# Optimization experiments

Hardware: AMD Instinct MI355X
Metric: run time of the kernel (lower is better)

## Reference

```python
import jax, jax.numpy as jnp
import numpy as np

B, S, D = 1, 4096, 1024
H, W = 16, 512            # heads, window_size
HD = D // H               # head_dim = 64


def setup_inputs() -> dict:
    key = jax.random.key(0)
    k1, k2, k3 = jax.random.split(key, 3)
    x = jax.random.normal(k1, (B, S, D), dtype=jnp.float32)
    w_qkv = jax.random.normal(k2, (D, 3 * D), dtype=jnp.float32) * 0.02
    w_out = jax.random.normal(k3, (D, D), dtype=jnp.float32) * 0.02
    return {"x": x, "w_qkv": w_qkv, "w_out": w_out}


def reference(x, w_qkv, w_out):
    b, s, d = x.shape
    qkv = x @ w_qkv                                   # [B,S,3D]
    q, k, v = jnp.split(qkv, 3, axis=-1)
    to_heads = lambda t: t.reshape(b, s, H, HD).transpose(0, 2, 1, 3)  # [B,H,S,hd]
    q, k, v = map(to_heads, (q, k, v))

    C = s // W                                        # number of chunks
    qc = q.reshape(b, H, C, W, HD)                    # [B,H,C,W,hd]
    kc = k.reshape(b, H, C, W, HD)
    vc = v.reshape(b, H, C, W, HD)

    # each chunk attends to [previous chunk, current chunk] of K/V (2W keys)
    zero = jnp.zeros_like(kc[:, :, :1])
    k_prev = jnp.concatenate([zero, kc[:, :, :-1]], axis=2)
    v_prev = jnp.concatenate([jnp.zeros_like(vc[:, :, :1]), vc[:, :, :-1]], axis=2)
    kcat = jnp.concatenate([k_prev, kc], axis=3)      # [B,H,C,2W,hd]
    vcat = jnp.concatenate([v_prev, vc], axis=3)

    scores = jnp.einsum('bhcqd,bhckd->bhcqk', qc, kcat) / (HD ** 0.5)

    # mask: causal (abs q_pos >= abs k_pos) and k_pos >= 0 (first chunk has no prev)
    wq = jnp.arange(W)
    jk = jnp.arange(2 * W)
    ci = jnp.arange(C)
    causal = (wq[:, None] + W) >= jk[None, :]                    # [W,2W]
    valid = (ci[:, None, None] * W + jk[None, None, :] - W) >= 0  # [C,1,2W]
    mask = causal[None] & valid                                   # [C,W,2W]

    scores = jnp.where(mask[None, None], scores, -jnp.inf)
    attn = jax.nn.softmax(scores, axis=-1)
    out = jnp.einsum('bhcqk,bhckd->bhcqd', attn, vcat)            # [B,H,C,W,hd]
    out = out.reshape(b, H, s, HD).transpose(0, 2, 1, 3).reshape(b, s, d)
    return out @ w_out
```

## Files before the change

### kernel.cpp

```cpp
#include <hip/hip_runtime.h>

typedef __attribute__((ext_vector_type(8))) short short8;
typedef __attribute__((ext_vector_type(4))) float f32x4;
typedef __attribute__((ext_vector_type(4))) unsigned short us4;
typedef unsigned short u16;

__device__ __forceinline__ u16 f2bf(float f) {
  unsigned int u = __float_as_uint(f);
  u += 0x7fffu + ((u >> 16) & 1u);
  return (u16)(u >> 16);
}

__device__ __forceinline__ void gld16(const void* g, void* l) {
  __builtin_amdgcn_global_load_lds((const __attribute__((address_space(1))) void*)g,
                                   (__attribute__((address_space(3))) void*)l, 16, 0, 0);
}

__global__ __launch_bounds__(256) void cast_f32_to_bf16(const float* __restrict__ in,
                                                        u16* __restrict__ out, int n8) {
  int i = blockIdx.x * 256 + threadIdx.x;
  if (i >= n8) return;
  const f32x4* p = (const f32x4*)in;
  f32x4 a = p[i * 2];
  f32x4 b = p[i * 2 + 1];
  short8 o;
#pragma unroll
  for (int j = 0; j < 4; ++j) o[j] = (short)f2bf(a[j]);
#pragma unroll
  for (int j = 0; j < 4; ++j) o[4 + j] = (short)f2bf(b[j]);
  ((short8*)out)[i] = o;
}

__global__ __launch_bounds__(256) void transpose_cast(const float* __restrict__ w,
                                                      u16* __restrict__ wT, int K, int N) {
  __shared__ float tile[32][33];
  int n0 = blockIdx.x * 32, k0 = blockIdx.y * 32;
  int r = threadIdx.x >> 5;
  int c = threadIdx.x & 31;
#pragma unroll
  for (int i = 0; i < 4; ++i)
    tile[r + i * 8][c] = w[(size_t)(k0 + r + i * 8) * N + n0 + c];
  __syncthreads();
#pragma unroll
  for (int i = 0; i < 4; ++i)
    wT[(size_t)(n0 + r + i * 8) * K + k0 + c] = f2bf(tile[c][r + i * 8]);
}

__global__ __launch_bounds__(256) void transpose_v(const u16* __restrict__ vh,
                                                   u16* __restrict__ vt) {
  __shared__ u16 tile[32][33];
  const int s0 = blockIdx.x * 32, d0 = blockIdx.y * 32, h = blockIdx.z;
  const long hb = (long)h * 4096 * 64;
  const long hb2 = (long)h * 64 * 4096;
  const int r = threadIdx.x >> 5, c = threadIdx.x & 31;
#pragma unroll
  for (int i = 0; i < 4; ++i)
    tile[r + i * 8][c] = vh[hb + (long)(s0 + r + i * 8) * 64 + d0 + c];
  __syncthreads();
#pragma unroll
  for (int i = 0; i < 4; ++i)
    vt[hb2 + (long)(d0 + r + i * 8) * 4096 + s0 + c] = tile[c][r + i * 8];
}

template <int MODE, int BM, int BN>
__global__ __launch_bounds__(256) void gemm_bf16(
    const u16* __restrict__ A, const u16* __restrict__ Bt, float* __restrict__ C,
    u16* __restrict__ q_out, u16* __restrict__ k_out, u16* __restrict__ v_out,
    int M, int N, int K) {
  __shared__ __align__(16) u16 As[BM][64];
  __shared__ __align__(16) u16 Bs[BN][64];
  constexpr int MW = BM / 32;
  constexpr int NW = BN / 32;
  const int t = threadIdx.x;
  const int lane = t & 63;
  const int wid = t >> 6;
  const int wm = wid >> 1, wn = wid & 1;
  const int l15 = lane & 15, lhi = lane >> 4;

  const int nbx = gridDim.x;
  const int bid = blockIdx.y * nbx + blockIdx.x;
  const int cpx = (nbx * gridDim.y) >> 3;
  const int wg = (bid & 7) * cpx + (bid >> 3);
  const int m0 = (wg / nbx) * BM;
  const int n0 = (wg % nbx) * BN;

  const int srow = lane >> 3;
  const int scol = ((lane & 7) ^ (lane >> 3)) * 8;

  f32x4 acc[MW][NW];
#pragma unroll
  for (int mi = 0; mi < MW; ++mi)
#pragma unroll
    for (int ni = 0; ni < NW; ++ni) acc[mi][ni] = (f32x4){0.f, 0.f, 0.f, 0.f};

  for (int k0 = 0; k0 < K; k0 += 64) {
    __syncthreads();
#pragma unroll
    for (int i = 0; i < MW; ++i) {
      int cch = wid * MW + i;
      int row = cch * 8 + srow;
      const u16* src = (MODE == 2)
          ? &A[((size_t)(k0 >> 6) * 4096 + m0 + row) * 64 + scol]
          : &A[(size_t)(m0 + row) * K + k0 + scol];
      gld16(src, &As[cch * 8][0]);
    }
#pragma unroll
    for (int i = 0; i < NW; ++i) {
      int cch = wid * NW + i;
      int row = cch * 8 + srow;
      gld16(&Bt[(size_t)(n0 + row) * K + k0 + scol], &Bs[cch * 8][0]);
    }
    __syncthreads();
#pragma unroll
    for (int kc = 0; kc < 2; ++kc) {
      short8 af[MW], bf[NW];
#pragma unroll
      for (int mi = 0; mi < MW; ++mi) {
        int row = wm * (BM / 2) + mi * 16 + l15;
        af[mi] = *(const short8*)&As[row][((kc * 4 + lhi) ^ (l15 & 7)) * 8];
      }
#pragma unroll
      for (int ni = 0; ni < NW; ++ni) {
        int row = wn * (BN / 2) + ni * 16 + l15;
        bf[ni] = *(const short8*)&Bs[row][((kc * 4 + lhi) ^ (l15 & 7)) * 8];
      }
#pragma unroll
      for (int mi = 0; mi < MW; ++mi)
#pragma unroll
        for (int ni = 0; ni < NW; ++ni)
          acc[mi][ni] = __builtin_amdgcn_mfma_f32_16x16x32_bf16(af[mi], bf[ni], acc[mi][ni], 0, 0, 0);
    }
  }

  const float SCQ = 0.18033688011112042f;
#pragma unroll
  for (int mi = 0; mi < MW; ++mi)
#pragma unroll
    for (int ni = 0; ni < NW; ++ni)
#pragma unroll
      for (int r = 0; r < 4; ++r) {
        int row = m0 + wm * (BM / 2) + mi * 16 + lhi * 4 + r;
        int col = n0 + wn * (BN / 2) + ni * 16 + l15;
        float val = acc[mi][ni][r];
        if constexpr (MODE == 1) {
          int which = col >> 10;
          int d = col & 1023;
          int hh = d >> 6, hd = d & 63;
          if (which == 0)      q_out[((size_t)hh * 4096 + row) * 64 + hd] = f2bf(val * SCQ);
          else if (which == 1) k_out[((size_t)hh * 4096 + row) * 64 + hd] = f2bf(val);
          else                 v_out[((size_t)hh * 4096 + row) * 64 + hd] = f2bf(val);
        } else {
          C[(size_t)row * N + col] = val;
        }
      }
}

__global__ __launch_bounds__(512) void attn_kernel(
    const u16* __restrict__ qh,
    const u16* __restrict__ kh,
    const u16* __restrict__ vt,
    u16* __restrict__ outh) {
  __shared__ __align__(16) u16 Ks[2][64][64];
  __shared__ __align__(16) u16 Vt[2][64][64];
  __shared__ __align__(16) unsigned int Pl[8][16][37];

  const int t = threadIdx.x;
  const int lane = t & 63;
  const int w = t >> 6;
  const int l15 = lane & 15;
  const int lhi = lane >> 4;

  const int bid = blockIdx.x;
  const int wk = (bid & 7) * 64 + (bid >> 3);
  const int qt = wk & 3, c = (wk >> 2) & 7, h = wk >> 5;

  const long head_base = (long)h * 4096 * 64;
  const int q0 = qt * 128;
  const long q_gbase = head_base + (long)(c * 512 + q0) * 64;

  short8 qf[2];
#pragma unroll
  for (int kc = 0; kc < 2; ++kc)
    qf[kc] = *(const short8*)&qh[q_gbase + (long)(w * 16 + l15) * 64 + kc * 32 + lhi * 8];

  float m_run = -1e30f, l_run = 0.f;
  f32x4 acc_o[4];
#pragma unroll
  for (int nd = 0; nd < 4; ++nd) acc_o[nd] = (f32x4){0.f, 0.f, 0.f, 0.f};

  const int kt_start = (c == 0) ? 8 : 0;
  const int kt_end = 2 * qt + 9;
  const long kv_base = head_base + ((long)c - 1) * 512 * 64;
  const long vt_hb = (long)h * 64 * 4096 + ((long)c - 1) * 512;

  const int srow = lane >> 3;
  const int sunit8 = ((lane & 7) ^ (lane >> 3)) * 8;

  {
    const int j0 = kt_start * 64;
    gld16(&kh[kv_base + (long)(j0 + w * 8 + srow) * 64 + sunit8], &Ks[0][w * 8][0]);
    gld16(&vt[vt_hb + (long)(w * 8 + srow) * 4096 + j0 + sunit8], &Vt[0][w * 8][0]);
  }
  __syncthreads();

  int cur = 0;
  for (int kt = kt_start; kt <= kt_end; ++kt) {
    const int j0 = kt * 64;
    const int nxt = cur ^ 1;

    if (kt < kt_end) {
      const int j0n = j0 + 64;
      gld16(&kh[kv_base + (long)(j0n + w * 8 + srow) * 64 + sunit8], &Ks[nxt][w * 8][0]);
      gld16(&vt[vt_hb + (long)(w * 8 + srow) * 4096 + j0n + sunit8], &Vt[nxt][w * 8][0]);
    }

    const bool active = (j0 <= q0 + w * 16 + 15 + 512);
    if (active) {
      f32x4 sa[4];
#pragma unroll
      for (int ni = 0; ni < 4; ++ni) sa[ni] = (f32x4){0.f, 0.f, 0.f, 0.f};
#pragma unroll
      for (int kc = 0; kc < 2; ++kc) {
        short8 kf[4];
#pragma unroll
        for (int ni = 0; ni < 4; ++ni) {
          int row = ni * 16 + l15;
          kf[ni] = *(const short8*)&Ks[cur][row][((kc * 4 + lhi) ^ (l15 & 7)) * 8];
        }
#pragma unroll
        for (int ni = 0; ni < 4; ++ni)
          sa[ni] = __builtin_amdgcn_mfma_f32_16x16x32_bf16(kf[ni], qf[kc], sa[ni], 0, 0, 0);
      }

      const int qloc = q0 + w * 16 + l15;
      if (j0 + 63 > q0 + w * 16 + 512) {
        const int lim = qloc + 512 - j0 - 4 * lhi;
#pragma unroll
        for (int ni = 0; ni < 4; ++ni)
#pragma unroll
          for (int r = 0; r < 4; ++r)
            if (16 * ni + r > lim) sa[ni][r] = -1e30f;
      }
      float v[16];
#pragma unroll
      for (int ni = 0; ni < 4; ++ni)
#pragma unroll
        for (int r = 0; r < 4; ++r) v[ni * 4 + r] = sa[ni][r];
#pragma unroll
      for (int s = 8; s >= 1; s >>= 1)
#pragma unroll
        for (int k = 0; k < s; ++k) v[k] = fmaxf(v[k], v[k + s]);
      float tm = v[0];
      tm = fmaxf(tm, __shfl_xor(tm, 16, 64));
      tm = fmaxf(tm, __shfl_xor(tm, 32, 64));

      float mn = fmaxf(m_run, tm);
      float corr = __builtin_amdgcn_exp2f(m_run - mn);
      m_run = mn;

      float ps[16];
#pragma unroll
      for (int ni = 0; ni < 4; ++ni) {
#pragma unroll
        for (int r = 0; r < 4; ++r) ps[ni * 4 + r] = __builtin_amdgcn_exp2f(sa[ni][r] - mn);
        unsigned int p01 = (unsigned int)f2bf(ps[ni * 4 + 0]) | ((unsigned int)f2bf(ps[ni * 4 + 1]) << 16);
        unsigned int p23 = (unsigned int)f2bf(ps[ni * 4 + 2]) | ((unsigned int)f2bf(ps[ni * 4 + 3]) << 16);
        Pl[w][l15][8 * ni + 2 * lhi + 0] = p01;
        Pl[w][l15][8 * ni + 2 * lhi + 1] = p23;
      }
#pragma unroll
      for (int s = 8; s >= 1; s >>= 1)
#pragma unroll
        for (int k = 0; k < s; ++k) ps[k] += ps[k + s];
      float ls = ps[0];
      ls += __shfl_xor(ls, 16, 64);
      ls += __shfl_xor(ls, 32, 64);
      l_run = l_run * corr + ls;
#pragma unroll
      for (int nd = 0; nd < 4; ++nd)
#pragma unroll
        for (int r = 0; r < 4; ++r) acc_o[nd][r] *= corr;

#pragma unroll
      for (int kc = 0; kc < 2; ++kc) {
        short8 pf = *(const short8*)&Pl[w][l15][kc * 16 + lhi * 4];
#pragma unroll
        for (int nd = 0; nd < 4; ++nd) {
          int row = nd * 16 + l15;
          short8 vf = *(const short8*)&Vt[cur][row][((kc * 4 + lhi) ^ (l15 & 7)) * 8];
          acc_o[nd] = __builtin_amdgcn_mfma_f32_16x16x32_bf16(vf, pf, acc_o[nd], 0, 0, 0);
        }
      }
    }
    __syncthreads();
    cur = nxt;
  }

  {
    float inv = 1.f / l_run;
    long s = (long)c * 512 + q0 + w * 16 + l15;
#pragma unroll
    for (int nd = 0; nd < 4; ++nd) {
      us4 o;
#pragma unroll
      for (int r = 0; r < 4; ++r) o[r] = f2bf(acc_o[nd][r] * inv);
      *(us4*)&outh[head_base + s * 64 + nd * 16 + lhi * 4] = o;
    }
  }
}

extern "C" void kernel_launch(void* const* d_in, const int* in_sizes, int n_in,
                              void* d_out, int out_size, void* d_ws, size_t ws_size,
                              hipStream_t stream) {
  const float* x = (const float*)d_in[0];
  const float* w_qkv = (const float*)d_in[1];
  const float* w_out = (const float*)d_in[2];
  float* out = (float*)d_out;

  u16* xb = (u16*)d_ws;
  u16* wqkvT = xb + 4096 * 1024;
  u16* woutT = wqkvT + 3072 * 1024;
  u16* qh = woutT + 1024 * 1024;
  u16* kh = qh + 16 * 4096 * 64;
  u16* vh = kh + 16 * 4096 * 64;
  u16* vt = xb;

  cast_f32_to_bf16<<<2048, 256, 0, stream>>>(x, xb, 4096 * 1024 / 8);
  transpose_cast<<<dim3(96, 32), 256, 0, stream>>>(w_qkv, wqkvT, 1024, 3072);
  transpose_cast<<<dim3(32, 32), 256, 0, stream>>>(w_out, woutT, 1024, 1024);

  gemm_bf16<1, 128, 128><<<dim3(24, 32), 256, 0, stream>>>(xb, wqkvT, nullptr, qh, kh, vh,
                                                           4096, 3072, 1024);
  transpose_v<<<dim3(128, 2, 16), 256, 0, stream>>>(vh, vt);
  attn_kernel<<<512, 512, 0, stream>>>(qh, kh, vt, qh);
  gemm_bf16<2, 64, 64><<<dim3(16, 64), 256, 0, stream>>>(qh, woutT, out, nullptr, nullptr, nullptr,
                                                         4096, 1024, 1024);
}
```

Baseline: 175.1 us.

## Merge prep kernels, add lazy softmax rescaling, retile output GEMM

Folds the x cast and both weight transpose-casts into one launch indexed by block id, which saves two kernel launches. In attention, the running max and the accumulator rescale are updated only when some lane's tile max exceeds the running max by more than a threshold. That skips the exp and multiply work on most iterations, at the cost of a wave-wide vote and a divergent branch. The output projection GEMM switches to 128x64 tiles, halving the grid.

```diff
diff --git a/kernel.cpp b/kernel.cpp
--- a/kernel.cpp
+++ b/kernel.cpp
@@ -16,34 +16,41 @@
                                    (__attribute__((address_space(3))) void*)l, 16, 0, 0);
 }
 
-__global__ __launch_bounds__(256) void cast_f32_to_bf16(const float* __restrict__ in,
-                                                        u16* __restrict__ out, int n8) {
-  int i = blockIdx.x * 256 + threadIdx.x;
-  if (i >= n8) return;
-  const f32x4* p = (const f32x4*)in;
-  f32x4 a = p[i * 2];
-  f32x4 b = p[i * 2 + 1];
-  short8 o;
-#pragma unroll
-  for (int j = 0; j < 4; ++j) o[j] = (short)f2bf(a[j]);
-#pragma unroll
-  for (int j = 0; j < 4; ++j) o[4 + j] = (short)f2bf(b[j]);
-  ((short8*)out)[i] = o;
-}
-
-__global__ __launch_bounds__(256) void transpose_cast(const float* __restrict__ w,
-                                                      u16* __restrict__ wT, int K, int N) {
+__global__ __launch_bounds__(256) void prep(
+    const float* __restrict__ x, u16* __restrict__ xb,
+    const float* __restrict__ wqkv, u16* __restrict__ wqkvT,
+    const float* __restrict__ wout, u16* __restrict__ woutT) {
   __shared__ float tile[32][33];
-  int n0 = blockIdx.x * 32, k0 = blockIdx.y * 32;
-  int r = threadIdx.x >> 5;
-  int c = threadIdx.x & 31;
-#pragma unroll
-  for (int i = 0; i < 4; ++i)
-    tile[r + i * 8][c] = w[(size_t)(k0 + r + i * 8) * N + n0 + c];
-  __syncthreads();
-#pragma unroll
-  for (int i = 0; i < 4; ++i)
-    wT[(size_t)(n0 + r + i * 8) * K + k0 + c] = f2bf(tile[c][r + i * 8]);
+  const int b = blockIdx.x;
+  const int t = threadIdx.x;
+  if (b < 2048) {
+    int i = b * 256 + t;
+    const f32x4* p = (const f32x4*)x;
+    f32x4 a = p[i * 2];
+    f32x4 bb = p[i * 2 + 1];
+    short8 o;
+#pragma unroll
+    for (int j = 0; j < 4; ++j) o[j] = (short)f2bf(a[j]);
+#pragma unroll
+    for (int j = 0; j < 4; ++j) o[4 + j] = (short)f2bf(bb[j]);
+    ((short8*)xb)[i] = o;
+  } else {
+    const float* src;
+    u16* dst;
+    int N, bb;
+    if (b < 5120) { bb = b - 2048; src = wqkv; dst = wqkvT; N = 3072; }
+    else          { bb = b - 5120; src = wout; dst = woutT; N = 1024; }
+    const int K = 1024, nb = N >> 5;
+    const int n0 = (bb % nb) * 32, k0 = (bb / nb) * 32;
+    const int r = t >> 5, c = t & 31;
+#pragma unroll
+    for (int i = 0; i < 4; ++i)
+      tile[r + i * 8][c] = src[(size_t)(k0 + r + i * 8) * N + n0 + c];
+    __syncthreads();
+#pragma unroll
+    for (int i = 0; i < 4; ++i)
+      dst[(size_t)(n0 + r + i * 8) * K + k0 + c] = f2bf(tile[c][r + i * 8]);
+  }
 }
 
 __global__ __launch_bounds__(256) void transpose_v(const u16* __restrict__ vh,
@@ -254,15 +261,19 @@
       tm = fmaxf(tm, __shfl_xor(tm, 16, 64));
       tm = fmaxf(tm, __shfl_xor(tm, 32, 64));
 
-      float mn = fmaxf(m_run, tm);
-      float corr = __builtin_amdgcn_exp2f(m_run - mn);
-      m_run = mn;
+      const bool resc = !__all(tm <= m_run + 8.0f);
+      float corr = 1.0f;
+      if (resc) {
+        float mn = fmaxf(m_run, tm);
+        corr = __builtin_amdgcn_exp2f(m_run - mn);
+        m_run = mn;
+      }
 
       float ps[16];
 #pragma unroll
       for (int ni = 0; ni < 4; ++ni) {
 #pragma unroll
-        for (int r = 0; r < 4; ++r) ps[ni * 4 + r] = __builtin_amdgcn_exp2f(sa[ni][r] - mn);
+        for (int r = 0; r < 4; ++r) ps[ni * 4 + r] = __builtin_amdgcn_exp2f(sa[ni][r] - m_run);
         unsigned int p01 = (unsigned int)f2bf(ps[ni * 4 + 0]) | ((unsigned int)f2bf(ps[ni * 4 + 1]) << 16);
         unsigned int p23 = (unsigned int)f2bf(ps[ni * 4 + 2]) | ((unsigned int)f2bf(ps[ni * 4 + 3]) << 16);
         Pl[w][l15][8 * ni + 2 * lhi + 0] = p01;
@@ -275,11 +286,15 @@
       float ls = ps[0];
       ls += __shfl_xor(ls, 16, 64);
       ls += __shfl_xor(ls, 32, 64);
-      l_run = l_run * corr + ls;
-#pragma unroll
-      for (int nd = 0; nd < 4; ++nd)
-#pragma unroll
-        for (int r = 0; r < 4; ++r) acc_o[nd][r] *= corr;
+      if (resc) {
+        l_run = l_run * corr + ls;
+#pragma unroll
+        for (int nd = 0; nd < 4; ++nd)
+#pragma unroll
+          for (int r = 0; r < 4; ++r) acc_o[nd][r] *= corr;
+      } else {
+        l_run += ls;
+      }
 
 #pragma unroll
       for (int kc = 0; kc < 2; ++kc) {
@@ -325,14 +340,11 @@
   u16* vh = kh + 16 * 4096 * 64;
   u16* vt = xb;
 
-  cast_f32_to_bf16<<<2048, 256, 0, stream>>>(x, xb, 4096 * 1024 / 8);
-  transpose_cast<<<dim3(96, 32), 256, 0, stream>>>(w_qkv, wqkvT, 1024, 3072);
-  transpose_cast<<<dim3(32, 32), 256, 0, stream>>>(w_out, woutT, 1024, 1024);
-
+  prep<<<6144, 256, 0, stream>>>(x, xb, w_qkv, wqkvT, w_out, woutT);
   gemm_bf16<1, 128, 128><<<dim3(24, 32), 256, 0, stream>>>(xb, wqkvT, nullptr, qh, kh, vh,
                                                            4096, 3072, 1024);
   transpose_v<<<dim3(128, 2, 16), 256, 0, stream>>>(vh, vt);
   attn_kernel<<<512, 512, 0, stream>>>(qh, kh, vt, qh);
-  gemm_bf16<2, 64, 64><<<dim3(16, 64), 256, 0, stream>>>(qh, woutT, out, nullptr, nullptr, nullptr,
-                                                         4096, 1024, 1024);
-}
+  gemm_bf16<2, 128, 64><<<dim3(16, 32), 256, 0, stream>>>(qh, woutT, out, nullptr, nullptr, nullptr,
+                                                          4096, 1024, 1024);
+}
```

New measurement: 177.4 us. About the same (+1.3%).
